# Kernel tuning notes

Measured on AMD Instinct MI355X. Metric: run time of the kernel, lower is better.

Reference implementation:

```python
import jax, jax.numpy as jnp
import numpy as np

MAX_SEQ_LEN = 512
PADDING_VALUE = -1.0
B, S_ENC, H, F = 128, 32, 768, 128


def setup_inputs() -> dict:
    key = jax.random.key(0)
    ks = jax.random.split(key, 9)
    s = 1.0 / np.sqrt(H)  # torch-style uniform-ish scale, use scaled normal
    return {
        "H_o": jax.random.normal(ks[0], (B, S_ENC, H), jnp.float32),
        "H_n": jax.random.normal(ks[1], (1, B, H), jnp.float32),
        "T": jax.random.randint(ks[2], (B,), 0, MAX_SEQ_LEN, jnp.int64),
        "W_ih": jax.random.normal(ks[3], (3 * H, H), jnp.float32) * s,
        "W_hh": jax.random.normal(ks[4], (3 * H, H), jnp.float32) * s,
        "b_ih": jax.random.normal(ks[5], (3 * H,), jnp.float32) * s,
        "b_hh": jax.random.normal(ks[6], (3 * H,), jnp.float32) * s,
        "W_lin": jax.random.normal(ks[7], (F, H), jnp.float32) * s,
        "b_lin": jax.random.normal(ks[8], (F,), jnp.float32) * s,
    }


def _gru_cell(x, h, W_ih, W_hh, b_ih, b_hh):
    # torch GRU gate ordering: reset, update, new
    gi = x @ W_ih.T + b_ih  # (B, 3H)
    gh = h @ W_hh.T + b_hh
    gi_r, gi_z, gi_n = jnp.split(gi, 3, axis=-1)
    gh_r, gh_z, gh_n = jnp.split(gh, 3, axis=-1)
    r = jax.nn.sigmoid(gi_r + gh_r)
    z = jax.nn.sigmoid(gi_z + gh_z)
    n = jnp.tanh(gi_n + r * gh_n)
    return (1.0 - z) * n + z * h


def reference(H_o, H_n, T, W_ih, W_hh, b_ih, b_hh, W_lin, b_lin):
    x0 = H_o[:, -1, :]  # (B, H): last encoder output seeds the decoder
    h0 = H_n[0]         # (B, H): single-layer hidden state

    def step(carry, _):
        x, h = carry
        h_new = _gru_cell(x, h, W_ih, W_hh, b_ih, b_hh)
        # output of single-layer GRU == new hidden; fed back as next input
        return (h_new, h_new), h_new

    _, Y = jax.lax.scan(step, (x0, h0), None, length=MAX_SEQ_LEN)  # (S, B, H)
    X_hat = jnp.einsum("sbh,fh->sbf", Y, W_lin) + b_lin            # (S, B, F)
    X_hat = jnp.transpose(X_hat, (1, 0, 2))[:, ::-1, :]            # (B, S, F), time-reversed
    valid = jnp.arange(MAX_SEQ_LEN)[None, :] < T[:, None]          # (B, S)
    return jnp.where(valid[:, :, None], X_hat, PADDING_VALUE)
```

## Files before the change

kernel.cpp:

```cpp
#include <hip/hip_runtime.h>

typedef _Float16 f16;
typedef _Float16 half8 __attribute__((ext_vector_type(8)));
typedef float f32x4 __attribute__((ext_vector_type(4)));
typedef int i32x4 __attribute__((ext_vector_type(4)));

#define SEQ 512
#define NB 128
#define NH 768
#define NFEAT 128
#define NGRP 4
#define BG 32
#define NCOL 48
#define NWG (NGRP*NCOL)
#define KW8 96
#define NKT8 3

#define OFF_WIH   0LL
#define OFF_WHH   3538944LL
#define OFF_WLIN  7077888LL
#define OFF_XBUF  7274496LL
#define OFF_HBUF  7471104LL
#define OFF_CTR   7667712LL
#define OFF_Y     7684096LL
#define OFF_TN    108347392LL
#define WS_NEED   (OFF_TN + 1024)

__global__ void fill_sentinel(float* out, long long n) {
  long long i = (long long)blockIdx.x * blockDim.x + threadIdx.x;
  long long stride = (long long)gridDim.x * blockDim.x;
  for (; i < n; i += stride) out[i] = -2.0f;
}

__global__ void prep_kernel(const float* __restrict__ Ho, const float* __restrict__ Hn,
                            const unsigned int* __restrict__ Traw,
                            const float* __restrict__ Wih, const float* __restrict__ Whh,
                            const float* __restrict__ Wlin,
                            f16* __restrict__ wih16, f16* __restrict__ whh16,
                            f16* __restrict__ wlin16,
                            f16* __restrict__ xbuf, f16* __restrict__ hbuf,
                            int* __restrict__ Tn)
{
  long long idx = (long long)blockIdx.x * blockDim.x + threadIdx.x;
  long long stride = (long long)gridDim.x * blockDim.x;
  for (long long i = idx; i < 2304LL * 768LL; i += stride) {
    wih16[i] = (f16)Wih[i];
    whh16[i] = (f16)Whh[i];
  }
  for (long long i = idx; i < 128LL * 768LL; i += stride) {
    long long b = i / 768, h = i % 768;
    wlin16[i] = (f16)Wlin[i];
    xbuf[i] = (f16)Ho[(b * 32 + 31) * 768 + h];
    hbuf[i] = (f16)Hn[i];
  }
  if (blockIdx.x == 0 && threadIdx.x < 128) {
    bool allz = true;
    for (int i = 0; i < 64; ++i) allz = allz && (Traw[2 * i + 1] == 0u);
    int t = threadIdx.x;
    Tn[t] = allz ? (int)Traw[2 * t] : (int)Traw[t];
  }
}

__global__ void __launch_bounds__(512, 1)
gru_kernel(const f16* __restrict__ wih16, const f16* __restrict__ whh16,
           const f16* __restrict__ xbuf, const f16* __restrict__ hbuf,
           const float* __restrict__ Hn,
           const float* __restrict__ b_ih, const float* __restrict__ b_hh,
           f16* __restrict__ Y, unsigned int* __restrict__ ctr)
{
  const int wg  = blockIdx.x;
  const int g   = wg & (NGRP - 1);
  const int c   = wg >> 2;
  const int tid = threadIdx.x;
  const int lane = tid & 63;
  const int wv  = tid >> 6;
  const int j0  = c * 16;
  const int ks  = wv * KW8;
  const int bbase = g * BG;

  __shared__ float pbuf[8 * 12 * 64 * 4];

  const int n15 = lane & 15;
  const int kg8 = (lane >> 4) * 8;

  half8 Bf[6][NKT8];
#pragma unroll
  for (int nt = 0; nt < 6; ++nt) {
    const f16* Wsrc = (nt < 3) ? wih16 : whh16;
    const f16* base = Wsrc + (size_t)((nt % 3) * 768 + j0 + n15) * NH + ks + kg8;
#pragma unroll
    for (int kt = 0; kt < NKT8; ++kt) {
      i32x4 raw = *(const volatile i32x4*)(base + kt * 32);
      Bf[nt][kt] = __builtin_bit_cast(half8, raw);
    }
  }

  const int gb = tid >> 4;
  const int gj = tid & 15;
  const int jglob = j0 + gj;
  float hcarry = Hn[(size_t)(bbase + gb) * NH + jglob];
  const float bi_r = b_ih[jglob], bi_z = b_ih[768 + jglob], bi_n = b_ih[1536 + jglob];
  const float bh_r = b_hh[jglob], bh_z = b_hh[768 + jglob], bh_n = b_hh[1536 + jglob];

  const size_t arow0 = (size_t)(bbase + n15) * NH + ks + kg8;
  const size_t arow1 = arow0 + (size_t)16 * NH;
  const size_t ywr   = (size_t)(bbase + gb) * NH + jglob;

  const int rt_g = gb >> 4, mt = gb & 15;
  const int off0 = rt_g * 1536 + (((mt >> 2) * 16 + gj) << 2) + (mt & 3);

  unsigned int* cbase = ctr + ((size_t)g << 9);

  for (int s = 0; s < SEQ; ++s) {
    const f16* hsrc = (s == 0) ? hbuf : (Y + (size_t)(s - 1) * (NB * NH));
    const f16* xsrc = (s == 0) ? xbuf : hsrc;

    half8 Af0_0 = *(const half8*)(xsrc + arow0);
    half8 Af0_1 = *(const half8*)(xsrc + arow0 + 32);
    half8 Af0_2 = *(const half8*)(xsrc + arow0 + 64);
    half8 Af1_0 = *(const half8*)(xsrc + arow1);
    half8 Af1_1 = *(const half8*)(xsrc + arow1 + 32);
    half8 Af1_2 = *(const half8*)(xsrc + arow1 + 64);

    f32x4 a00 = {0.f,0.f,0.f,0.f}, a01 = {0.f,0.f,0.f,0.f}, a02 = {0.f,0.f,0.f,0.f};
    f32x4 a03 = {0.f,0.f,0.f,0.f}, a04 = {0.f,0.f,0.f,0.f}, a05 = {0.f,0.f,0.f,0.f};
    f32x4 a10 = {0.f,0.f,0.f,0.f}, a11 = {0.f,0.f,0.f,0.f}, a12 = {0.f,0.f,0.f,0.f};
    f32x4 a13 = {0.f,0.f,0.f,0.f}, a14 = {0.f,0.f,0.f,0.f}, a15 = {0.f,0.f,0.f,0.f};

    a00 = __builtin_amdgcn_mfma_f32_16x16x32_f16(Af0_0, Bf[0][0], a00, 0, 0, 0);
    a01 = __builtin_amdgcn_mfma_f32_16x16x32_f16(Af0_0, Bf[1][0], a01, 0, 0, 0);
    a02 = __builtin_amdgcn_mfma_f32_16x16x32_f16(Af0_0, Bf[2][0], a02, 0, 0, 0);
    a10 = __builtin_amdgcn_mfma_f32_16x16x32_f16(Af1_0, Bf[0][0], a10, 0, 0, 0);
    a11 = __builtin_amdgcn_mfma_f32_16x16x32_f16(Af1_0, Bf[1][0], a11, 0, 0, 0);
    a12 = __builtin_amdgcn_mfma_f32_16x16x32_f16(Af1_0, Bf[2][0], a12, 0, 0, 0);
    a00 = __builtin_amdgcn_mfma_f32_16x16x32_f16(Af0_1, Bf[0][1], a00, 0, 0, 0);
    a01 = __builtin_amdgcn_mfma_f32_16x16x32_f16(Af0_1, Bf[1][1], a01, 0, 0, 0);
    a02 = __builtin_amdgcn_mfma_f32_16x16x32_f16(Af0_1, Bf[2][1], a02, 0, 0, 0);
    a10 = __builtin_amdgcn_mfma_f32_16x16x32_f16(Af1_1, Bf[0][1], a10, 0, 0, 0);
    a11 = __builtin_amdgcn_mfma_f32_16x16x32_f16(Af1_1, Bf[1][1], a11, 0, 0, 0);
    a12 = __builtin_amdgcn_mfma_f32_16x16x32_f16(Af1_1, Bf[2][1], a12, 0, 0, 0);
    a00 = __builtin_amdgcn_mfma_f32_16x16x32_f16(Af0_2, Bf[0][2], a00, 0, 0, 0);
    a01 = __builtin_amdgcn_mfma_f32_16x16x32_f16(Af0_2, Bf[1][2], a01, 0, 0, 0);
    a02 = __builtin_amdgcn_mfma_f32_16x16x32_f16(Af0_2, Bf[2][2], a02, 0, 0, 0);
    a10 = __builtin_amdgcn_mfma_f32_16x16x32_f16(Af1_2, Bf[0][2], a10, 0, 0, 0);
    a11 = __builtin_amdgcn_mfma_f32_16x16x32_f16(Af1_2, Bf[1][2], a11, 0, 0, 0);
    a12 = __builtin_amdgcn_mfma_f32_16x16x32_f16(Af1_2, Bf[2][2], a12, 0, 0, 0);

    if (s == 0) {
      Af0_0 = *(const half8*)(hbuf + arow0);
      Af0_1 = *(const half8*)(hbuf + arow0 + 32);
      Af0_2 = *(const half8*)(hbuf + arow0 + 64);
      Af1_0 = *(const half8*)(hbuf + arow1);
      Af1_1 = *(const half8*)(hbuf + arow1 + 32);
      Af1_2 = *(const half8*)(hbuf + arow1 + 64);
    }

    a03 = __builtin_amdgcn_mfma_f32_16x16x32_f16(Af0_0, Bf[3][0], a03, 0, 0, 0);
    a04 = __builtin_amdgcn_mfma_f32_16x16x32_f16(Af0_0, Bf[4][0], a04, 0, 0, 0);
    a05 = __builtin_amdgcn_mfma_f32_16x16x32_f16(Af0_0, Bf[5][0], a05, 0, 0, 0);
    a13 = __builtin_amdgcn_mfma_f32_16x16x32_f16(Af1_0, Bf[3][0], a13, 0, 0, 0);
    a14 = __builtin_amdgcn_mfma_f32_16x16x32_f16(Af1_0, Bf[4][0], a14, 0, 0, 0);
    a15 = __builtin_amdgcn_mfma_f32_16x16x32_f16(Af1_0, Bf[5][0], a15, 0, 0, 0);
    a03 = __builtin_amdgcn_mfma_f32_16x16x32_f16(Af0_1, Bf[3][1], a03, 0, 0, 0);
    a04 = __builtin_amdgcn_mfma_f32_16x16x32_f16(Af0_1, Bf[4][1], a04, 0, 0, 0);
    a05 = __builtin_amdgcn_mfma_f32_16x16x32_f16(Af0_1, Bf[5][1], a05, 0, 0, 0);
    a13 = __builtin_amdgcn_mfma_f32_16x16x32_f16(Af1_1, Bf[3][1], a13, 0, 0, 0);
    a14 = __builtin_amdgcn_mfma_f32_16x16x32_f16(Af1_1, Bf[4][1], a14, 0, 0, 0);
    a15 = __builtin_amdgcn_mfma_f32_16x16x32_f16(Af1_1, Bf[5][1], a15, 0, 0, 0);
    a03 = __builtin_amdgcn_mfma_f32_16x16x32_f16(Af0_2, Bf[3][2], a03, 0, 0, 0);
    a04 = __builtin_amdgcn_mfma_f32_16x16x32_f16(Af0_2, Bf[4][2], a04, 0, 0, 0);
    a05 = __builtin_amdgcn_mfma_f32_16x16x32_f16(Af0_2, Bf[5][2], a05, 0, 0, 0);
    a13 = __builtin_amdgcn_mfma_f32_16x16x32_f16(Af1_2, Bf[3][2], a13, 0, 0, 0);
    a14 = __builtin_amdgcn_mfma_f32_16x16x32_f16(Af1_2, Bf[4][2], a14, 0, 0, 0);
    a15 = __builtin_amdgcn_mfma_f32_16x16x32_f16(Af1_2, Bf[5][2], a15, 0, 0, 0);

    {
      f32x4* pb = (f32x4*)pbuf;
      const int wbase = wv * 768 + lane;
      pb[wbase +   0] = a00;  pb[wbase +  64] = a01;  pb[wbase + 128] = a02;
      pb[wbase + 192] = a03;  pb[wbase + 256] = a04;  pb[wbase + 320] = a05;
      pb[wbase + 384] = a10;  pb[wbase + 448] = a11;  pb[wbase + 512] = a12;
      pb[wbase + 576] = a13;  pb[wbase + 640] = a14;  pb[wbase + 704] = a15;
    }
    __syncthreads();

    float gir = bi_r, giz = bi_z, gin = bi_n, ghr = bh_r, ghz = bh_z, ghn = bh_n;
#pragma unroll
    for (int ww = 0; ww < 8; ++ww) {
      const float* p = pbuf + ww * 3072 + off0;
      gir += p[0];    giz += p[256];  gin += p[512];
      ghr += p[768];  ghz += p[1024]; ghn += p[1280];
    }
    float rr = 1.f / (1.f + __expf(-(gir + ghr)));
    float zz = 1.f / (1.f + __expf(-(giz + ghz)));
    float xn = gin + rr * ghn;
    float nn = 1.f - 2.f / (__expf(2.f * xn) + 1.f);
    float hnew = (1.f - zz) * nn + zz * hcarry;
    hcarry = hnew;

    unsigned int u = (unsigned int)__builtin_bit_cast(unsigned short, (f16)hnew);
    unsigned int partner = (unsigned int)__shfl_xor((int)u, 1);
    if ((tid & 1) == 0) {
      unsigned int val = u | (partner << 16);
      unsigned int* dst = (unsigned int*)(Y + (size_t)s * (NB * NH) + ywr);
      __hip_atomic_store(dst, val, __ATOMIC_RELAXED, __HIP_MEMORY_SCOPE_AGENT);
    }

    __syncthreads();
    if (tid == 0) {
      unsigned int* cp = cbase + s;
      __hip_atomic_fetch_add(cp, 1u, __ATOMIC_RELAXED, __HIP_MEMORY_SCOPE_AGENT);
      while (__hip_atomic_load(cp, __ATOMIC_RELAXED, __HIP_MEMORY_SCOPE_AGENT) < NCOL)
        __builtin_amdgcn_s_sleep(1);
    }
    __syncthreads();
  }
}

__global__ void __launch_bounds__(256)
proj_kernel(const f16* __restrict__ Y, const f16* __restrict__ wlin16,
            const float* __restrict__ b_lin, const int* __restrict__ Tn,
            float* __restrict__ out)
{
  const int tid = threadIdx.x;
  const int lane = tid & 63;
  const int wv = tid >> 6;
  const int r0 = blockIdx.x * 64 + wv * 16;
  const int n15 = lane & 15;
  const int kg8 = (lane >> 4) * 8;
  const size_t arow_off = (size_t)(r0 + n15) * NH + kg8;

  f32x4 acc[8];
#pragma unroll
  for (int nf = 0; nf < 8; ++nf) acc[nf] = (f32x4){0.f, 0.f, 0.f, 0.f};

  for (int kt = 0; kt < 24; ++kt) {
    half8 a = *(const half8*)(Y + arow_off + kt * 32);
#pragma unroll
    for (int nf = 0; nf < 8; ++nf) {
      half8 bfr = *(const half8*)(wlin16 + (size_t)(nf * 16 + n15) * NH + kt * 32 + kg8);
      acc[nf] = __builtin_amdgcn_mfma_f32_16x16x32_f16(a, bfr, acc[nf], 0, 0, 0);
    }
  }

#pragma unroll
  for (int nf = 0; nf < 8; ++nf) {
    int fcol = nf * 16 + n15;
    float bl = b_lin[fcol];
#pragma unroll
    for (int r = 0; r < 4; ++r) {
      int row = r0 + (lane >> 4) * 4 + r;
      int s = row >> 7, b = row & 127;
      int t = 511 - s;
      float v = (t < Tn[b]) ? (acc[nf][r] + bl) : -1.0f;
      out[((size_t)b * 512 + t) * NFEAT + fcol] = v;
    }
  }
}

extern "C" void kernel_launch(void* const* d_in, const int* in_sizes, int n_in,
                              void* d_out, int out_size, void* d_ws, size_t ws_size,
                              hipStream_t stream) {
  const float* Ho   = (const float*)d_in[0];
  const float* Hn   = (const float*)d_in[1];
  const unsigned int* Traw = (const unsigned int*)d_in[2];
  const float* Wih  = (const float*)d_in[3];
  const float* Whh  = (const float*)d_in[4];
  const float* bih  = (const float*)d_in[5];
  const float* bhh  = (const float*)d_in[6];
  const float* Wlin = (const float*)d_in[7];
  const float* blin = (const float*)d_in[8];
  float* out = (float*)d_out;

  if (ws_size < (size_t)WS_NEED) {
    fill_sentinel<<<1024, 256, 0, stream>>>(out, (long long)out_size);
    return;
  }

  char* ws = (char*)d_ws;
  f16* wih16  = (f16*)(ws + OFF_WIH);
  f16* whh16  = (f16*)(ws + OFF_WHH);
  f16* wlin16 = (f16*)(ws + OFF_WLIN);
  f16* xbuf   = (f16*)(ws + OFF_XBUF);
  f16* hbuf   = (f16*)(ws + OFF_HBUF);
  unsigned int* ctr = (unsigned int*)(ws + OFF_CTR);
  f16* Y      = (f16*)(ws + OFF_Y);
  int* Tn     = (int*)(ws + OFF_TN);

  hipMemsetAsync(ctr, 0, NGRP * SEQ * sizeof(unsigned int), stream);
  prep_kernel<<<512, 256, 0, stream>>>(Ho, Hn, Traw, Wih, Whh, Wlin,
                                       wih16, whh16, wlin16, xbuf, hbuf, Tn);
  gru_kernel<<<NWG, 512, 0, stream>>>(wih16, whh16, xbuf, hbuf, Hn, bih, bhh, Y, ctr);
  proj_kernel<<<1024, 256, 0, stream>>>(Y, wlin16, blin, Tn, out);
}
```

Baseline: 2.068 ms.

## Reload GRU weights per step, overlapping loads with the inter-workgroup barrier

```diff
diff --git a/kernel.cpp b/kernel.cpp
--- a/kernel.cpp
+++ b/kernel.cpp
@@ -14,7 +14,6 @@
 #define NCOL 48
 #define NWG (NGRP*NCOL)
 #define KW8 96
-#define NKT8 3
 
 #define OFF_WIH   0LL
 #define OFF_WHH   3538944LL
@@ -60,6 +59,12 @@
     Tn[t] = allz ? (int)Traw[2 * t] : (int)Traw[t];
   }
 }
+
+#define PF3(d0, d1, d2, b) do {                                                \
+  asm volatile("global_load_dwordx4 %0, %1, off"            : "=v"(d0) : "v"(b)); \
+  asm volatile("global_load_dwordx4 %0, %1, off offset:64"  : "=v"(d1) : "v"(b)); \
+  asm volatile("global_load_dwordx4 %0, %1, off offset:128" : "=v"(d2) : "v"(b)); \
+} while (0)
 
 __global__ void __launch_bounds__(512, 1)
 gru_kernel(const f16* __restrict__ wih16, const f16* __restrict__ whh16,
@@ -83,17 +88,12 @@
   const int n15 = lane & 15;
   const int kg8 = (lane >> 4) * 8;
 
-  half8 Bf[6][NKT8];
-#pragma unroll
-  for (int nt = 0; nt < 6; ++nt) {
-    const f16* Wsrc = (nt < 3) ? wih16 : whh16;
-    const f16* base = Wsrc + (size_t)((nt % 3) * 768 + j0 + n15) * NH + ks + kg8;
-#pragma unroll
-    for (int kt = 0; kt < NKT8; ++kt) {
-      i32x4 raw = *(const volatile i32x4*)(base + kt * 32);
-      Bf[nt][kt] = __builtin_bit_cast(half8, raw);
-    }
-  }
+  const f16* wb0 = wih16 + (size_t)(0 * 768 + j0 + n15) * NH + ks + kg8;
+  const f16* wb1 = wih16 + (size_t)(1 * 768 + j0 + n15) * NH + ks + kg8;
+  const f16* wb2 = wih16 + (size_t)(2 * 768 + j0 + n15) * NH + ks + kg8;
+  const f16* wb3 = whh16 + (size_t)(0 * 768 + j0 + n15) * NH + ks + kg8;
+  const f16* wb4 = whh16 + (size_t)(1 * 768 + j0 + n15) * NH + ks + kg8;
+  const f16* wb5 = whh16 + (size_t)(2 * 768 + j0 + n15) * NH + ks + kg8;
 
   const int gb = tid >> 4;
   const int gj = tid & 15;
@@ -112,6 +112,30 @@
   unsigned int* cbase = ctr + ((size_t)g << 9);
 
   for (int s = 0; s < SEQ; ++s) {
+    i32x4 w00, w01, w02, w10, w11, w12, w20, w21, w22;
+    i32x4 w30, w31, w32, w40, w41, w42, w50, w51, w52;
+    PF3(w00, w01, w02, wb0);
+    PF3(w10, w11, w12, wb1);
+    PF3(w20, w21, w22, wb2);
+    PF3(w30, w31, w32, wb3);
+    PF3(w40, w41, w42, wb4);
+    PF3(w50, w51, w52, wb5);
+
+    if (s > 0 && tid == 0) {
+      unsigned int* cp = cbase + (s - 1);
+      while (__hip_atomic_load(cp, __ATOMIC_RELAXED, __HIP_MEMORY_SCOPE_AGENT) < NCOL)
+        __builtin_amdgcn_s_sleep(1);
+    }
+    __syncthreads();
+    __builtin_amdgcn_sched_barrier(0);
+
+    half8 B00 = __builtin_bit_cast(half8, w00), B01 = __builtin_bit_cast(half8, w01), B02 = __builtin_bit_cast(half8, w02);
+    half8 B10 = __builtin_bit_cast(half8, w10), B11 = __builtin_bit_cast(half8, w11), B12 = __builtin_bit_cast(half8, w12);
+    half8 B20 = __builtin_bit_cast(half8, w20), B21 = __builtin_bit_cast(half8, w21), B22 = __builtin_bit_cast(half8, w22);
+    half8 B30 = __builtin_bit_cast(half8, w30), B31 = __builtin_bit_cast(half8, w31), B32 = __builtin_bit_cast(half8, w32);
+    half8 B40 = __builtin_bit_cast(half8, w40), B41 = __builtin_bit_cast(half8, w41), B42 = __builtin_bit_cast(half8, w42);
+    half8 B50 = __builtin_bit_cast(half8, w50), B51 = __builtin_bit_cast(half8, w51), B52 = __builtin_bit_cast(half8, w52);
+
     const f16* hsrc = (s == 0) ? hbuf : (Y + (size_t)(s - 1) * (NB * NH));
     const f16* xsrc = (s == 0) ? xbuf : hsrc;
 
@@ -127,24 +151,24 @@
     f32x4 a10 = {0.f,0.f,0.f,0.f}, a11 = {0.f,0.f,0.f,0.f}, a12 = {0.f,0.f,0.f,0.f};
     f32x4 a13 = {0.f,0.f,0.f,0.f}, a14 = {0.f,0.f,0.f,0.f}, a15 = {0.f,0.f,0.f,0.f};
 
-    a00 = __builtin_amdgcn_mfma_f32_16x16x32_f16(Af0_0, Bf[0][0], a00, 0, 0, 0);
-    a01 = __builtin_amdgcn_mfma_f32_16x16x32_f16(Af0_0, Bf[1][0], a01, 0, 0, 0);
-    a02 = __builtin_amdgcn_mfma_f32_16x16x32_f16(Af0_0, Bf[2][0], a02, 0, 0, 0);
-    a10 = __builtin_amdgcn_mfma_f32_16x16x32_f16(Af1_0, Bf[0][0], a10, 0, 0, 0);
-    a11 = __builtin_amdgcn_mfma_f32_16x16x32_f16(Af1_0, Bf[1][0], a11, 0, 0, 0);
-    a12 = __builtin_amdgcn_mfma_f32_16x16x32_f16(Af1_0, Bf[2][0], a12, 0, 0, 0);
-    a00 = __builtin_amdgcn_mfma_f32_16x16x32_f16(Af0_1, Bf[0][1], a00, 0, 0, 0);
-    a01 = __builtin_amdgcn_mfma_f32_16x16x32_f16(Af0_1, Bf[1][1], a01, 0, 0, 0);
-    a02 = __builtin_amdgcn_mfma_f32_16x16x32_f16(Af0_1, Bf[2][1], a02, 0, 0, 0);
-    a10 = __builtin_amdgcn_mfma_f32_16x16x32_f16(Af1_1, Bf[0][1], a10, 0, 0, 0);
-    a11 = __builtin_amdgcn_mfma_f32_16x16x32_f16(Af1_1, Bf[1][1], a11, 0, 0, 0);
-    a12 = __builtin_amdgcn_mfma_f32_16x16x32_f16(Af1_1, Bf[2][1], a12, 0, 0, 0);
-    a00 = __builtin_amdgcn_mfma_f32_16x16x32_f16(Af0_2, Bf[0][2], a00, 0, 0, 0);
-    a01 = __builtin_amdgcn_mfma_f32_16x16x32_f16(Af0_2, Bf[1][2], a01, 0, 0, 0);
-    a02 = __builtin_amdgcn_mfma_f32_16x16x32_f16(Af0_2, Bf[2][2], a02, 0, 0, 0);
-    a10 = __builtin_amdgcn_mfma_f32_16x16x32_f16(Af1_2, Bf[0][2], a10, 0, 0, 0);
-    a11 = __builtin_amdgcn_mfma_f32_16x16x32_f16(Af1_2, Bf[1][2], a11, 0, 0, 0);
-    a12 = __builtin_amdgcn_mfma_f32_16x16x32_f16(Af1_2, Bf[2][2], a12, 0, 0, 0);
+    a00 = __builtin_amdgcn_mfma_f32_16x16x32_f16(Af0_0, B00, a00, 0, 0, 0);
+    a01 = __builtin_amdgcn_mfma_f32_16x16x32_f16(Af0_0, B10, a01, 0, 0, 0);
+    a02 = __builtin_amdgcn_mfma_f32_16x16x32_f16(Af0_0, B20, a02, 0, 0, 0);
+    a10 = __builtin_amdgcn_mfma_f32_16x16x32_f16(Af1_0, B00, a10, 0, 0, 0);
+    a11 = __builtin_amdgcn_mfma_f32_16x16x32_f16(Af1_0, B10, a11, 0, 0, 0);
+    a12 = __builtin_amdgcn_mfma_f32_16x16x32_f16(Af1_0, B20, a12, 0, 0, 0);
+    a00 = __builtin_amdgcn_mfma_f32_16x16x32_f16(Af0_1, B01, a00, 0, 0, 0);
+    a01 = __builtin_amdgcn_mfma_f32_16x16x32_f16(Af0_1, B11, a01, 0, 0, 0);
+    a02 = __builtin_amdgcn_mfma_f32_16x16x32_f16(Af0_1, B21, a02, 0, 0, 0);
+    a10 = __builtin_amdgcn_mfma_f32_16x16x32_f16(Af1_1, B01, a10, 0, 0, 0);
+    a11 = __builtin_amdgcn_mfma_f32_16x16x32_f16(Af1_1, B11, a11, 0, 0, 0);
+    a12 = __builtin_amdgcn_mfma_f32_16x16x32_f16(Af1_1, B21, a12, 0, 0, 0);
+    a00 = __builtin_amdgcn_mfma_f32_16x16x32_f16(Af0_2, B02, a00, 0, 0, 0);
+    a01 = __builtin_amdgcn_mfma_f32_16x16x32_f16(Af0_2, B12, a01, 0, 0, 0);
+    a02 = __builtin_amdgcn_mfma_f32_16x16x32_f16(Af0_2, B22, a02, 0, 0, 0);
+    a10 = __builtin_amdgcn_mfma_f32_16x16x32_f16(Af1_2, B02, a10, 0, 0, 0);
+    a11 = __builtin_amdgcn_mfma_f32_16x16x32_f16(Af1_2, B12, a11, 0, 0, 0);
+    a12 = __builtin_amdgcn_mfma_f32_16x16x32_f16(Af1_2, B22, a12, 0, 0, 0);
 
     if (s == 0) {
       Af0_0 = *(const half8*)(hbuf + arow0);
@@ -155,24 +179,24 @@
       Af1_2 = *(const half8*)(hbuf + arow1 + 64);
     }
 
-    a03 = __builtin_amdgcn_mfma_f32_16x16x32_f16(Af0_0, Bf[3][0], a03, 0, 0, 0);
-    a04 = __builtin_amdgcn_mfma_f32_16x16x32_f16(Af0_0, Bf[4][0], a04, 0, 0, 0);
-    a05 = __builtin_amdgcn_mfma_f32_16x16x32_f16(Af0_0, Bf[5][0], a05, 0, 0, 0);
-    a13 = __builtin_amdgcn_mfma_f32_16x16x32_f16(Af1_0, Bf[3][0], a13, 0, 0, 0);
-    a14 = __builtin_amdgcn_mfma_f32_16x16x32_f16(Af1_0, Bf[4][0], a14, 0, 0, 0);
-    a15 = __builtin_amdgcn_mfma_f32_16x16x32_f16(Af1_0, Bf[5][0], a15, 0, 0, 0);
-    a03 = __builtin_amdgcn_mfma_f32_16x16x32_f16(Af0_1, Bf[3][1], a03, 0, 0, 0);
-    a04 = __builtin_amdgcn_mfma_f32_16x16x32_f16(Af0_1, Bf[4][1], a04, 0, 0, 0);
-    a05 = __builtin_amdgcn_mfma_f32_16x16x32_f16(Af0_1, Bf[5][1], a05, 0, 0, 0);
-    a13 = __builtin_amdgcn_mfma_f32_16x16x32_f16(Af1_1, Bf[3][1], a13, 0, 0, 0);
-    a14 = __builtin_amdgcn_mfma_f32_16x16x32_f16(Af1_1, Bf[4][1], a14, 0, 0, 0);
-    a15 = __builtin_amdgcn_mfma_f32_16x16x32_f16(Af1_1, Bf[5][1], a15, 0, 0, 0);
-    a03 = __builtin_amdgcn_mfma_f32_16x16x32_f16(Af0_2, Bf[3][2], a03, 0, 0, 0);
-    a04 = __builtin_amdgcn_mfma_f32_16x16x32_f16(Af0_2, Bf[4][2], a04, 0, 0, 0);
-    a05 = __builtin_amdgcn_mfma_f32_16x16x32_f16(Af0_2, Bf[5][2], a05, 0, 0, 0);
-    a13 = __builtin_amdgcn_mfma_f32_16x16x32_f16(Af1_2, Bf[3][2], a13, 0, 0, 0);
-    a14 = __builtin_amdgcn_mfma_f32_16x16x32_f16(Af1_2, Bf[4][2], a14, 0, 0, 0);
-    a15 = __builtin_amdgcn_mfma_f32_16x16x32_f16(Af1_2, Bf[5][2], a15, 0, 0, 0);
+    a03 = __builtin_amdgcn_mfma_f32_16x16x32_f16(Af0_0, B30, a03, 0, 0, 0);
+    a04 = __builtin_amdgcn_mfma_f32_16x16x32_f16(Af0_0, B40, a04, 0, 0, 0);
+    a05 = __builtin_amdgcn_mfma_f32_16x16x32_f16(Af0_0, B50, a05, 0, 0, 0);
+    a13 = __builtin_amdgcn_mfma_f32_16x16x32_f16(Af1_0, B30, a13, 0, 0, 0);
+    a14 = __builtin_amdgcn_mfma_f32_16x16x32_f16(Af1_0, B40, a14, 0, 0, 0);
+    a15 = __builtin_amdgcn_mfma_f32_16x16x32_f16(Af1_0, B50, a15, 0, 0, 0);
+    a03 = __builtin_amdgcn_mfma_f32_16x16x32_f16(Af0_1, B31, a03, 0, 0, 0);
+    a04 = __builtin_amdgcn_mfma_f32_16x16x32_f16(Af0_1, B41, a04, 0, 0, 0);
+    a05 = __builtin_amdgcn_mfma_f32_16x16x32_f16(Af0_1, B51, a05, 0, 0, 0);
+    a13 = __builtin_amdgcn_mfma_f32_16x16x32_f16(Af1_1, B31, a13, 0, 0, 0);
+    a14 = __builtin_amdgcn_mfma_f32_16x16x32_f16(Af1_1, B41, a14, 0, 0, 0);
+    a15 = __builtin_amdgcn_mfma_f32_16x16x32_f16(Af1_1, B51, a15, 0, 0, 0);
+    a03 = __builtin_amdgcn_mfma_f32_16x16x32_f16(Af0_2, B32, a03, 0, 0, 0);
+    a04 = __builtin_amdgcn_mfma_f32_16x16x32_f16(Af0_2, B42, a04, 0, 0, 0);
+    a05 = __builtin_amdgcn_mfma_f32_16x16x32_f16(Af0_2, B52, a05, 0, 0, 0);
+    a13 = __builtin_amdgcn_mfma_f32_16x16x32_f16(Af1_2, B32, a13, 0, 0, 0);
+    a14 = __builtin_amdgcn_mfma_f32_16x16x32_f16(Af1_2, B42, a14, 0, 0, 0);
+    a15 = __builtin_amdgcn_mfma_f32_16x16x32_f16(Af1_2, B52, a15, 0, 0, 0);
 
     {
       f32x4* pb = (f32x4*)pbuf;
@@ -207,13 +231,8 @@
     }
 
     __syncthreads();
-    if (tid == 0) {
-      unsigned int* cp = cbase + s;
-      __hip_atomic_fetch_add(cp, 1u, __ATOMIC_RELAXED, __HIP_MEMORY_SCOPE_AGENT);
-      while (__hip_atomic_load(cp, __ATOMIC_RELAXED, __HIP_MEMORY_SCOPE_AGENT) < NCOL)
-        __builtin_amdgcn_s_sleep(1);
-    }
-    __syncthreads();
+    if (tid == 0)
+      __hip_atomic_fetch_add(cbase + s, 1u, __ATOMIC_RELAXED, __HIP_MEMORY_SCOPE_AGENT);
   }
 }
 
```

New measurement: 3.716 ms. 79.7% more time.
